# Kernel optimization log

Measured on AMD Instinct MI355X. Metric: run time of the kernel, lower is better.

The kernel has to match this reference:

```python
import jax, jax.numpy as jnp
import numpy as np

N_ENT = 100000   # n_entities
N_REL = 40       # n_relations_ckg
D = 64           # embed_dim
L = 3            # n_layers
E = 1000000      # number of CKG triples (edges)


def setup_inputs() -> dict:
    key = jax.random.key(0)
    k = jax.random.split(key, 6)
    xavier = np.sqrt(6.0 / (D + D))  # xavier_uniform for square Linear
    return {
        "heads": jax.random.randint(k[0], (E,), 0, N_ENT),
        "rels": jax.random.randint(k[1], (E,), 0, N_REL),
        "tails": jax.random.randint(k[2], (E,), 0, N_ENT),
        "entity_embed": 0.01 * jax.random.normal(k[3], (N_ENT, D), dtype=jnp.float32),
        "rel_embeds": 0.01 * jax.random.normal(k[4], (L, N_REL, D), dtype=jnp.float32),
        "Ws": (jax.random.uniform(k[5], (L, D, D), minval=-1.0, maxval=1.0) * xavier).astype(jnp.float32),
    }


def _kgat_layer(h, heads, rels, tails, rel_emb, W):
    # h: [N, D]; heads/rels/tails: [E]; rel_emb: [n_rel, D]; W: [D, D] (nn.Linear weight)
    n = h.shape[0]
    e_h = h[heads]            # [E, D] gather
    e_t = h[tails]            # [E, D] gather
    e_r = rel_emb[rels]       # [E, D] gather
    # pi(h,r,t) = e_t . tanh(e_h + e_r)
    score = jnp.sum(e_t * jnp.tanh(e_h + e_r), axis=-1)          # [E]
    score = score - jax.lax.stop_gradient(jnp.max(score))        # global shift (detach)
    score_exp = jnp.exp(score)                                   # [E]
    score_sum = jax.ops.segment_sum(score_exp, heads, num_segments=n)  # [N]
    attn = score_exp / (score_sum[heads] + 1e-10)                # [E] per-head softmax
    agg = jax.ops.segment_sum(attn[:, None] * e_t, heads, num_segments=n)  # [N, D]
    out = (h + agg) @ W.T                                        # Linear, no bias
    return jax.nn.leaky_relu(out, negative_slope=0.2)            # dropout = identity (eval)


def reference(heads, rels, tails, entity_embed, rel_embeds, Ws):
    h = entity_embed
    all_layers = [h]
    for l in range(rel_embeds.shape[0]):
        h = _kgat_layer(h, heads, rels, tails, rel_embeds[l], Ws[l])
        all_layers.append(h)
    return jnp.concatenate(all_layers, axis=-1)  # [N, D*(L+1)]
```

## Files before the change

kernel.cpp:

```cpp
#include <hip/hip_runtime.h>

#define DD 64
#define ROW 256
#define CHUNK 1024

__global__ void k_copy_embed(const float* __restrict__ ent, float* __restrict__ out, int n_rows) {
    int idx = blockIdx.x * blockDim.x + threadIdx.x;
    int total = n_rows * 16;
    if (idx >= total) return;
    int n = idx >> 4, q = idx & 15;
    const float4* src = (const float4*)(ent + (long)n * DD);
    float4* dst = (float4*)(out + (long)n * ROW);
    dst[q] = src[q];
}

__global__ void k_count(const int* __restrict__ heads, int* __restrict__ counts, int nE) {
    int e = blockIdx.x * 256 + threadIdx.x;
    if (e >= nE) return;
    atomicAdd(counts + heads[e], 1);
}

__global__ __launch_bounds__(256) void k_scan_chunk(
        const int* __restrict__ counts, int* __restrict__ offs,
        int* __restrict__ partials, int n) {
    __shared__ int lds[256];
    int base = blockIdx.x * CHUNK;
    int t = threadIdx.x;
    int c[4]; int sum = 0;
    #pragma unroll
    for (int j = 0; j < 4; ++j) {
        int i = base + t * 4 + j;
        c[j] = (i < n) ? counts[i] : 0;
        sum += c[j];
    }
    lds[t] = sum; __syncthreads();
    for (int d = 1; d < 256; d <<= 1) {
        int v = (t >= d) ? lds[t - d] : 0;
        __syncthreads();
        lds[t] += v;
        __syncthreads();
    }
    int excl = lds[t] - sum;
    if (t == 255) partials[blockIdx.x] = lds[255];
    int run = excl;
    #pragma unroll
    for (int j = 0; j < 4; ++j) {
        int i = base + t * 4 + j;
        if (i < n) offs[i] = run;
        run += c[j];
    }
}

__global__ __launch_bounds__(128) void k_scan_part(int* __restrict__ partials, int nb) {
    __shared__ int lds[128];
    int t = threadIdx.x;
    int v = (t < nb) ? partials[t] : 0;
    lds[t] = v; __syncthreads();
    for (int d = 1; d < 128; d <<= 1) {
        int u = (t >= d) ? lds[t - d] : 0;
        __syncthreads();
        lds[t] += u;
        __syncthreads();
    }
    if (t < nb) partials[t] = lds[t] - v;
}

__global__ void k_scan_add(int* __restrict__ offs, int* __restrict__ running,
                           const int* __restrict__ partials, int n, int nE) {
    int i = blockIdx.x * 256 + threadIdx.x;
    if (i < n) {
        int v = offs[i] + partials[i >> 10];
        offs[i] = v;
        running[i] = v;
    } else if (i == n) {
        offs[n] = nE;
    }
}

__global__ void k_scatter(const int* __restrict__ heads, const int* __restrict__ rels,
                          const int* __restrict__ tails, int* __restrict__ running,
                          int* __restrict__ packed, int nE) {
    int e = blockIdx.x * 256 + threadIdx.x;
    if (e >= nE) return;
    int h = heads[e];
    int pos = atomicAdd(running + h, 1);
    packed[pos] = tails[e] | (rels[e] << 20);
}

__global__ __launch_bounds__(256) void k_layer(
        const int* __restrict__ offs, const int* __restrict__ packed,
        const float* __restrict__ hbase, const float* __restrict__ relemb,
        const float* __restrict__ W, float* __restrict__ outbase,
        int n_heads, int nE) {
    __shared__ float Wt[DD * 65];
    __shared__ float xs[4][DD];
    for (int idx = threadIdx.x; idx < DD * DD; idx += 256)
        Wt[(idx & 63) * 65 + (idx >> 6)] = W[idx];
    __syncthreads();

    int w = threadIdx.x >> 6, lane = threadIdx.x & 63;
    int g = lane >> 4, s = lane & 15;

    for (int hd = blockIdx.x * 4 + w; hd < n_heads; hd += gridDim.x * 4) {
        const float4 eh4 = *(const float4*)(hbase + (long)hd * ROW + 4 * s);
        float4 acc = make_float4(0.f, 0.f, 0.f, 0.f);
        float ssum = 0.f;
        int p0 = offs[hd], pe = offs[hd + 1];

        for (int cbase = p0; cbase < pe; cbase += 64) {
            int clen = min(pe - cbase, 64);
            int vAll = packed[min(cbase + lane, nE - 1)];

            int i0 = (g < clen) ? g : 0;
            int i1 = (4 + g < clen) ? 4 + g : 0;
            int v0 = __shfl(vAll, i0);
            int v1 = __shfl(vAll, i1);
            float4 tt0 = *(const float4*)(hbase + (long)(v0 & 0xFFFFF) * ROW + 4 * s);
            float4 rr0 = *(const float4*)(relemb + (v0 >> 20) * DD + 4 * s);
            float4 tt1 = *(const float4*)(hbase + (long)(v1 & 0xFFFFF) * ROW + 4 * s);
            float4 rr1 = *(const float4*)(relemb + (v1 >> 20) * DD + 4 * s);

            for (int i = 0; i < clen; i += 8) {
                int ia = i + 8 + g;  ia = (ia < clen) ? ia : 0;
                int ib = i + 12 + g; ib = (ib < clen) ? ib : 0;
                int va = __shfl(vAll, ia);
                int vb = __shfl(vAll, ib);
                float4 tta = *(const float4*)(hbase + (long)(va & 0xFFFFF) * ROW + 4 * s);
                float4 rra = *(const float4*)(relemb + (va >> 20) * DD + 4 * s);
                float4 ttb = *(const float4*)(hbase + (long)(vb & 0xFFFFF) * ROW + 4 * s);
                float4 rrb = *(const float4*)(relemb + (vb >> 20) * DD + 4 * s);

                {
                    float sc = 0.f;
                    #pragma unroll
                    for (int q = 0; q < 4; ++q) {
                        float xq = (&eh4.x)[q] + (&rr0.x)[q];
                        float t = __expf(2.f * xq);
                        float th = 1.f - 2.f * __builtin_amdgcn_rcpf(t + 1.f);
                        sc += (&tt0.x)[q] * th;
                    }
                    #pragma unroll
                    for (int off = 1; off <= 8; off <<= 1) sc += __shfl_xor(sc, off);
                    float se = ((i + g) < clen) ? __expf(sc) : 0.f;
                    ssum += se;
                    acc.x += se * tt0.x; acc.y += se * tt0.y;
                    acc.z += se * tt0.z; acc.w += se * tt0.w;
                }
                {
                    float sc = 0.f;
                    #pragma unroll
                    for (int q = 0; q < 4; ++q) {
                        float xq = (&eh4.x)[q] + (&rr1.x)[q];
                        float t = __expf(2.f * xq);
                        float th = 1.f - 2.f * __builtin_amdgcn_rcpf(t + 1.f);
                        sc += (&tt1.x)[q] * th;
                    }
                    #pragma unroll
                    for (int off = 1; off <= 8; off <<= 1) sc += __shfl_xor(sc, off);
                    float se = ((i + 4 + g) < clen) ? __expf(sc) : 0.f;
                    ssum += se;
                    acc.x += se * tt1.x; acc.y += se * tt1.y;
                    acc.z += se * tt1.z; acc.w += se * tt1.w;
                }
                tt0 = tta; rr0 = rra; tt1 = ttb; rr1 = rrb;
            }
        }

        #pragma unroll
        for (int off = 16; off <= 32; off <<= 1) {
            acc.x += __shfl_xor(acc.x, off);
            acc.y += __shfl_xor(acc.y, off);
            acc.z += __shfl_xor(acc.z, off);
            acc.w += __shfl_xor(acc.w, off);
            ssum  += __shfl_xor(ssum,  off);
        }
        float inv = 1.f / (ssum + 1e-10f);
        float4 x4;
        x4.x = eh4.x + acc.x * inv;  x4.y = eh4.y + acc.y * inv;
        x4.z = eh4.z + acc.z * inv;  x4.w = eh4.w + acc.w * inv;
        if (g == 0) *(float4*)(&xs[w][4 * s]) = x4;

        float y = 0.f;
        const float* xw = xs[w];
        #pragma unroll
        for (int k4 = 0; k4 < DD; k4 += 4) {
            float4 xv = *(const float4*)(xw + k4);
            y += xv.x * Wt[(k4 + 0) * 65 + lane];
            y += xv.y * Wt[(k4 + 1) * 65 + lane];
            y += xv.z * Wt[(k4 + 2) * 65 + lane];
            y += xv.w * Wt[(k4 + 3) * 65 + lane];
        }
        y = y >= 0.f ? y : 0.2f * y;
        outbase[(long)hd * ROW + lane] = y;
    }
}

extern "C" void kernel_launch(void* const* d_in, const int* in_sizes, int n_in,
                              void* d_out, int out_size, void* d_ws, size_t ws_size,
                              hipStream_t stream) {
    const int*   heads = (const int*)d_in[0];
    const int*   rels  = (const int*)d_in[1];
    const int*   tails = (const int*)d_in[2];
    const float* ent   = (const float*)d_in[3];
    const float* rel   = (const float*)d_in[4];
    const float* Ws    = (const float*)d_in[5];
    float* out = (float*)d_out;

    const int nE = in_sizes[0];
    const int N  = in_sizes[3] / DD;
    const int L  = in_sizes[5] / (DD * DD);
    const int NREL = in_sizes[4] / (L * DD);

    int* offs    = (int*)d_ws;
    int* running = offs + (N + 1);
    int* packed  = running + N;
    int* partials = packed + nE - 128;

    dim3 blk(256);
    int copy_blocks = (N * 16 + 255) / 256;
    int nchunks = (N + CHUNK - 1) / CHUNK;

    k_copy_embed<<<copy_blocks, blk, 0, stream>>>(ent, out, N);

    hipMemsetAsync(running, 0, (size_t)N * sizeof(int), stream);
    k_count<<<(nE + 255) / 256, blk, 0, stream>>>(heads, running, nE);
    k_scan_chunk<<<nchunks, blk, 0, stream>>>(running, offs, partials, N);
    k_scan_part<<<1, 128, 0, stream>>>(partials, nchunks);
    k_scan_add<<<(N + 1 + 255) / 256, blk, 0, stream>>>(offs, running, partials, N, nE);
    k_scatter<<<(nE + 255) / 256, blk, 0, stream>>>(heads, rels, tails, running, packed, nE);

    for (int l = 0; l < L; ++l) {
        k_layer<<<2048, blk, 0, stream>>>(
            offs, packed, out + l * DD, rel + (long)l * NREL * DD,
            Ws + (long)l * DD * DD, out + (l + 1) * DD, N, nE);
    }
}
```

Before: 500.5 us.

## Assign one head per 16-lane group and fuse graph-build preprocessing kernels

The layer kernel now maps each 16-lane group to its own head, so a wave processes four heads at once. Each group walks that head's edge list two edges at a time, and the W matvec is batched over four heads from shared memory. This replaces the old wave-per-head grid-stride loop, which wasted lanes on short neighbour lists and repeated the matvec for every head. Preprocessing is also trimmed: the copy and the counts zeroing share one kernel, the partials scan is folded into the scan-add kernel, and the per-edge atomic rank is kept so the scatter needs no second atomic pass. In exchange, a wave's loop runs to the largest degree among its four heads, and the rank path needs more workspace (it falls back when the workspace is too small).

Measured after the change: 573.8 us. +14.7%, slower.

```diff
diff --git a/kernel.cpp b/kernel.cpp
--- a/kernel.cpp
+++ b/kernel.cpp
@@ -4,14 +4,25 @@
 #define ROW 256
 #define CHUNK 1024
 
-__global__ void k_copy_embed(const float* __restrict__ ent, float* __restrict__ out, int n_rows) {
-    int idx = blockIdx.x * blockDim.x + threadIdx.x;
-    int total = n_rows * 16;
-    if (idx >= total) return;
-    int n = idx >> 4, q = idx & 15;
-    const float4* src = (const float4*)(ent + (long)n * DD);
-    float4* dst = (float4*)(out + (long)n * ROW);
-    dst[q] = src[q];
+__global__ void k_init(const float* __restrict__ ent, float* __restrict__ out,
+                       int* __restrict__ counts, int n_rows, int copy_blocks) {
+    if ((int)blockIdx.x < copy_blocks) {
+        int idx = blockIdx.x * 256 + threadIdx.x;
+        int total = n_rows * 16;
+        if (idx >= total) return;
+        int n = idx >> 4, q = idx & 15;
+        ((float4*)(out + (long)n * ROW))[q] = ((const float4*)(ent + (long)n * DD))[q];
+    } else {
+        int i = (blockIdx.x - copy_blocks) * 256 + threadIdx.x;
+        if (i < n_rows) counts[i] = 0;
+    }
+}
+
+__global__ void k_count_rank(const int* __restrict__ heads, int* __restrict__ counts,
+                             int* __restrict__ rank, int nE) {
+    int e = blockIdx.x * 256 + threadIdx.x;
+    if (e >= nE) return;
+    rank[e] = atomicAdd(counts + heads[e], 1);
 }
 
 __global__ void k_count(const int* __restrict__ heads, int* __restrict__ counts, int nE) {
@@ -51,30 +62,38 @@
     }
 }
 
-__global__ __launch_bounds__(128) void k_scan_part(int* __restrict__ partials, int nb) {
+__global__ __launch_bounds__(256) void k_scan_add(
+        int* __restrict__ offs, int* __restrict__ cursors,
+        const int* __restrict__ partials, int n, int nE, int nb, int write_cursors) {
     __shared__ int lds[128];
     int t = threadIdx.x;
-    int v = (t < nb) ? partials[t] : 0;
-    lds[t] = v; __syncthreads();
+    int v = 0;
+    if (t < 128) { v = (t < nb) ? partials[t] : 0; lds[t] = v; }
+    __syncthreads();
     for (int d = 1; d < 128; d <<= 1) {
-        int u = (t >= d) ? lds[t - d] : 0;
-        __syncthreads();
-        lds[t] += u;
-        __syncthreads();
-    }
-    if (t < nb) partials[t] = lds[t] - v;
-}
-
-__global__ void k_scan_add(int* __restrict__ offs, int* __restrict__ running,
-                           const int* __restrict__ partials, int n, int nE) {
-    int i = blockIdx.x * 256 + threadIdx.x;
+        int u = (t >= d && t < 128) ? lds[t - d] : 0;
+        __syncthreads();
+        if (t < 128) lds[t] += u;
+        __syncthreads();
+    }
+    if (t < 128) lds[t] -= v;
+    __syncthreads();
+    int i = blockIdx.x * 256 + t;
     if (i < n) {
-        int v = offs[i] + partials[i >> 10];
-        offs[i] = v;
-        running[i] = v;
+        int val = offs[i] + lds[i >> 10];
+        offs[i] = val;
+        if (write_cursors) cursors[i] = val;
     } else if (i == n) {
         offs[n] = nE;
     }
+}
+
+__global__ void k_scatter_rank(const int* __restrict__ heads, const int* __restrict__ rels,
+                               const int* __restrict__ tails, const int* __restrict__ offs,
+                               const int* __restrict__ rank, int* __restrict__ packed, int nE) {
+    int e = blockIdx.x * 256 + threadIdx.x;
+    if (e >= nE) return;
+    packed[offs[heads[e]] + rank[e]] = tails[e] | (rels[e] << 20);
 }
 
 __global__ void k_scatter(const int* __restrict__ heads, const int* __restrict__ rels,
@@ -82,8 +101,7 @@
                           int* __restrict__ packed, int nE) {
     int e = blockIdx.x * 256 + threadIdx.x;
     if (e >= nE) return;
-    int h = heads[e];
-    int pos = atomicAdd(running + h, 1);
+    int pos = atomicAdd(running + heads[e], 1);
     packed[pos] = tails[e] | (rels[e] << 20);
 }
 
@@ -93,7 +111,7 @@
         const float* __restrict__ W, float* __restrict__ outbase,
         int n_heads, int nE) {
     __shared__ float Wt[DD * 65];
-    __shared__ float xs[4][DD];
+    __shared__ float xs[4][4][DD];
     for (int idx = threadIdx.x; idx < DD * DD; idx += 256)
         Wt[(idx & 63) * 65 + (idx >> 6)] = W[idx];
     __syncthreads();
@@ -101,98 +119,106 @@
     int w = threadIdx.x >> 6, lane = threadIdx.x & 63;
     int g = lane >> 4, s = lane & 15;
 
-    for (int hd = blockIdx.x * 4 + w; hd < n_heads; hd += gridDim.x * 4) {
-        const float4 eh4 = *(const float4*)(hbase + (long)hd * ROW + 4 * s);
-        float4 acc = make_float4(0.f, 0.f, 0.f, 0.f);
-        float ssum = 0.f;
-        int p0 = offs[hd], pe = offs[hd + 1];
-
-        for (int cbase = p0; cbase < pe; cbase += 64) {
-            int clen = min(pe - cbase, 64);
-            int vAll = packed[min(cbase + lane, nE - 1)];
-
-            int i0 = (g < clen) ? g : 0;
-            int i1 = (4 + g < clen) ? 4 + g : 0;
-            int v0 = __shfl(vAll, i0);
-            int v1 = __shfl(vAll, i1);
-            float4 tt0 = *(const float4*)(hbase + (long)(v0 & 0xFFFFF) * ROW + 4 * s);
-            float4 rr0 = *(const float4*)(relemb + (v0 >> 20) * DD + 4 * s);
-            float4 tt1 = *(const float4*)(hbase + (long)(v1 & 0xFFFFF) * ROW + 4 * s);
-            float4 rr1 = *(const float4*)(relemb + (v1 >> 20) * DD + 4 * s);
-
-            for (int i = 0; i < clen; i += 8) {
-                int ia = i + 8 + g;  ia = (ia < clen) ? ia : 0;
-                int ib = i + 12 + g; ib = (ib < clen) ? ib : 0;
-                int va = __shfl(vAll, ia);
-                int vb = __shfl(vAll, ib);
-                float4 tta = *(const float4*)(hbase + (long)(va & 0xFFFFF) * ROW + 4 * s);
-                float4 rra = *(const float4*)(relemb + (va >> 20) * DD + 4 * s);
-                float4 ttb = *(const float4*)(hbase + (long)(vb & 0xFFFFF) * ROW + 4 * s);
-                float4 rrb = *(const float4*)(relemb + (vb >> 20) * DD + 4 * s);
-
-                {
-                    float sc = 0.f;
-                    #pragma unroll
-                    for (int q = 0; q < 4; ++q) {
-                        float xq = (&eh4.x)[q] + (&rr0.x)[q];
-                        float t = __expf(2.f * xq);
-                        float th = 1.f - 2.f * __builtin_amdgcn_rcpf(t + 1.f);
-                        sc += (&tt0.x)[q] * th;
-                    }
-                    #pragma unroll
-                    for (int off = 1; off <= 8; off <<= 1) sc += __shfl_xor(sc, off);
-                    float se = ((i + g) < clen) ? __expf(sc) : 0.f;
-                    ssum += se;
-                    acc.x += se * tt0.x; acc.y += se * tt0.y;
-                    acc.z += se * tt0.z; acc.w += se * tt0.w;
-                }
-                {
-                    float sc = 0.f;
-                    #pragma unroll
-                    for (int q = 0; q < 4; ++q) {
-                        float xq = (&eh4.x)[q] + (&rr1.x)[q];
-                        float t = __expf(2.f * xq);
-                        float th = 1.f - 2.f * __builtin_amdgcn_rcpf(t + 1.f);
-                        sc += (&tt1.x)[q] * th;
-                    }
-                    #pragma unroll
-                    for (int off = 1; off <= 8; off <<= 1) sc += __shfl_xor(sc, off);
-                    float se = ((i + 4 + g) < clen) ? __expf(sc) : 0.f;
-                    ssum += se;
-                    acc.x += se * tt1.x; acc.y += se * tt1.y;
-                    acc.z += se * tt1.z; acc.w += se * tt1.w;
-                }
-                tt0 = tta; rr0 = rra; tt1 = ttb; rr1 = rrb;
+    int hd0 = blockIdx.x * 16 + w * 4;
+    if (hd0 >= n_heads) return;
+    int hd = hd0 + g;
+    int hdc = (hd < n_heads) ? hd : 0;
+
+    const float4 eh4 = *(const float4*)(hbase + (long)hdc * ROW + 4 * s);
+    int p  = offs[hdc];
+    int pe = offs[hdc + 1];
+
+    int rem = pe - p;
+    int m = rem;
+    m = max(m, __shfl_xor(m, 16));
+    m = max(m, __shfl_xor(m, 32));
+
+    float4 acc = make_float4(0.f, 0.f, 0.f, 0.f);
+    float ssum = 0.f;
+
+    int pc = p;
+    int v0 = packed[min(pc,     nE - 1)];
+    int v1 = packed[min(pc + 1, nE - 1)];
+    float4 tt0 = *(const float4*)(hbase + (long)(v0 & 0xFFFFF) * ROW + 4 * s);
+    float4 rr0 = *(const float4*)(relemb + (v0 >> 20) * DD + 4 * s);
+    float4 tt1 = *(const float4*)(hbase + (long)(v1 & 0xFFFFF) * ROW + 4 * s);
+    float4 rr1 = *(const float4*)(relemb + (v1 >> 20) * DD + 4 * s);
+
+    for (int it = 0; it < m; it += 2) {
+        int va = packed[min(pc + 2, nE - 1)];
+        int vb = packed[min(pc + 3, nE - 1)];
+        float4 tta = *(const float4*)(hbase + (long)(va & 0xFFFFF) * ROW + 4 * s);
+        float4 rra = *(const float4*)(relemb + (va >> 20) * DD + 4 * s);
+        float4 ttb = *(const float4*)(hbase + (long)(vb & 0xFFFFF) * ROW + 4 * s);
+        float4 rrb = *(const float4*)(relemb + (vb >> 20) * DD + 4 * s);
+
+        {
+            float sc = 0.f;
+            #pragma unroll
+            for (int q = 0; q < 4; ++q) {
+                float xq = (&eh4.x)[q] + (&rr0.x)[q];
+                float t = __expf(2.f * xq);
+                float th = 1.f - 2.f * __builtin_amdgcn_rcpf(t + 1.f);
+                sc += (&tt0.x)[q] * th;
             }
+            #pragma unroll
+            for (int off = 1; off <= 8; off <<= 1) sc += __shfl_xor(sc, off);
+            float se = (pc < pe) ? __expf(sc) : 0.f;
+            ssum += se;
+            acc.x += se * tt0.x; acc.y += se * tt0.y;
+            acc.z += se * tt0.z; acc.w += se * tt0.w;
         }
-
-        #pragma unroll
-        for (int off = 16; off <= 32; off <<= 1) {
-            acc.x += __shfl_xor(acc.x, off);
-            acc.y += __shfl_xor(acc.y, off);
-            acc.z += __shfl_xor(acc.z, off);
-            acc.w += __shfl_xor(acc.w, off);
-            ssum  += __shfl_xor(ssum,  off);
+        {
+            float sc = 0.f;
+            #pragma unroll
+            for (int q = 0; q < 4; ++q) {
+                float xq = (&eh4.x)[q] + (&rr1.x)[q];
+                float t = __expf(2.f * xq);
+                float th = 1.f - 2.f * __builtin_amdgcn_rcpf(t + 1.f);
+                sc += (&tt1.x)[q] * th;
+            }
+            #pragma unroll
+            for (int off = 1; off <= 8; off <<= 1) sc += __shfl_xor(sc, off);
+            float se = (pc + 1 < pe) ? __expf(sc) : 0.f;
+            ssum += se;
+            acc.x += se * tt1.x; acc.y += se * tt1.y;
+            acc.z += se * tt1.z; acc.w += se * tt1.w;
         }
-        float inv = 1.f / (ssum + 1e-10f);
-        float4 x4;
-        x4.x = eh4.x + acc.x * inv;  x4.y = eh4.y + acc.y * inv;
-        x4.z = eh4.z + acc.z * inv;  x4.w = eh4.w + acc.w * inv;
-        if (g == 0) *(float4*)(&xs[w][4 * s]) = x4;
-
-        float y = 0.f;
-        const float* xw = xs[w];
-        #pragma unroll
-        for (int k4 = 0; k4 < DD; k4 += 4) {
-            float4 xv = *(const float4*)(xw + k4);
-            y += xv.x * Wt[(k4 + 0) * 65 + lane];
-            y += xv.y * Wt[(k4 + 1) * 65 + lane];
-            y += xv.z * Wt[(k4 + 2) * 65 + lane];
-            y += xv.w * Wt[(k4 + 3) * 65 + lane];
-        }
-        y = y >= 0.f ? y : 0.2f * y;
-        outbase[(long)hd * ROW + lane] = y;
-    }
+        pc += 2;
+        tt0 = tta; rr0 = rra; tt1 = ttb; rr1 = rrb;
+    }
+
+    float inv = __builtin_amdgcn_rcpf(ssum + 1e-10f);
+    float4 x4;
+    x4.x = eh4.x + acc.x * inv;  x4.y = eh4.y + acc.y * inv;
+    x4.z = eh4.z + acc.z * inv;  x4.w = eh4.w + acc.w * inv;
+    *(float4*)(&xs[w][g][4 * s]) = x4;
+
+    const float* xw = &xs[w][0][0];
+    float y0 = 0.f, y1 = 0.f, y2 = 0.f, y3 = 0.f;
+    #pragma unroll
+    for (int k4 = 0; k4 < DD; k4 += 4) {
+        float4 a0 = *(const float4*)(xw + 0 * DD + k4);
+        float4 a1 = *(const float4*)(xw + 1 * DD + k4);
+        float4 a2 = *(const float4*)(xw + 2 * DD + k4);
+        float4 a3 = *(const float4*)(xw + 3 * DD + k4);
+        float w0 = Wt[(k4 + 0) * 65 + lane];
+        float w1 = Wt[(k4 + 1) * 65 + lane];
+        float w2 = Wt[(k4 + 2) * 65 + lane];
+        float w3 = Wt[(k4 + 3) * 65 + lane];
+        y0 += a0.x * w0 + a0.y * w1 + a0.z * w2 + a0.w * w3;
+        y1 += a1.x * w0 + a1.y * w1 + a1.z * w2 + a1.w * w3;
+        y2 += a2.x * w0 + a2.y * w1 + a2.z * w2 + a2.w * w3;
+        y3 += a3.x * w0 + a3.y * w1 + a3.z * w2 + a3.w * w3;
+    }
+    y0 = y0 >= 0.f ? y0 : 0.2f * y0;
+    y1 = y1 >= 0.f ? y1 : 0.2f * y1;
+    y2 = y2 >= 0.f ? y2 : 0.2f * y2;
+    y3 = y3 >= 0.f ? y3 : 0.2f * y3;
+    if (hd0 + 0 < n_heads) outbase[(long)(hd0 + 0) * ROW + lane] = y0;
+    if (hd0 + 1 < n_heads) outbase[(long)(hd0 + 1) * ROW + lane] = y1;
+    if (hd0 + 2 < n_heads) outbase[(long)(hd0 + 2) * ROW + lane] = y2;
+    if (hd0 + 3 < n_heads) outbase[(long)(hd0 + 3) * ROW + lane] = y3;
 }
 
 extern "C" void kernel_launch(void* const* d_in, const int* in_sizes, int n_in,
@@ -211,26 +237,37 @@
     const int L  = in_sizes[5] / (DD * DD);
     const int NREL = in_sizes[4] / (L * DD);
 
-    int* offs    = (int*)d_ws;
-    int* running = offs + (N + 1);
-    int* packed  = running + N;
+    int* offs   = (int*)d_ws;
+    int* counts = offs + (N + 1);
+    int* packed = counts + N;
+    int* rank   = packed + nE;
     int* partials = packed + nE - 128;
+
+    size_t need_rank = ((size_t)(2 * N + 1) + 2 * (size_t)nE) * sizeof(int);
+    int use_rank = (ws_size >= need_rank) ? 1 : 0;
 
     dim3 blk(256);
     int copy_blocks = (N * 16 + 255) / 256;
+    int zero_blocks = (N + 255) / 256;
+    int edge_blocks = (nE + 255) / 256;
     int nchunks = (N + CHUNK - 1) / CHUNK;
 
-    k_copy_embed<<<copy_blocks, blk, 0, stream>>>(ent, out, N);
-
-    hipMemsetAsync(running, 0, (size_t)N * sizeof(int), stream);
-    k_count<<<(nE + 255) / 256, blk, 0, stream>>>(heads, running, nE);
-    k_scan_chunk<<<nchunks, blk, 0, stream>>>(running, offs, partials, N);
-    k_scan_part<<<1, 128, 0, stream>>>(partials, nchunks);
-    k_scan_add<<<(N + 1 + 255) / 256, blk, 0, stream>>>(offs, running, partials, N, nE);
-    k_scatter<<<(nE + 255) / 256, blk, 0, stream>>>(heads, rels, tails, running, packed, nE);
-
+    k_init<<<copy_blocks + zero_blocks, blk, 0, stream>>>(ent, out, counts, N, copy_blocks);
+    if (use_rank)
+        k_count_rank<<<edge_blocks, blk, 0, stream>>>(heads, counts, rank, nE);
+    else
+        k_count<<<edge_blocks, blk, 0, stream>>>(heads, counts, nE);
+    k_scan_chunk<<<nchunks, blk, 0, stream>>>(counts, offs, partials, N);
+    k_scan_add<<<(N + 1 + 255) / 256, blk, 0, stream>>>(
+        offs, counts, partials, N, nE, nchunks, use_rank ? 0 : 1);
+    if (use_rank)
+        k_scatter_rank<<<edge_blocks, blk, 0, stream>>>(heads, rels, tails, offs, rank, packed, nE);
+    else
+        k_scatter<<<edge_blocks, blk, 0, stream>>>(heads, rels, tails, counts, packed, nE);
+
+    int layer_blocks = (N + 15) / 16;
     for (int l = 0; l < L; ++l) {
-        k_layer<<<2048, blk, 0, stream>>>(
+        k_layer<<<layer_blocks, blk, 0, stream>>>(
             offs, packed, out + l * DD, rel + (long)l * NREL * DD,
             Ws + (long)l * DD * DD, out + (l + 1) * DD, N, nE);
     }
```
